# Optimization experiments

Measured on AMD Instinct MI355X. Metric: run time of the kernel, lower is better.

The kernel has to match this reference:

```python
import jax, jax.numpy as jnp
import numpy as np

HEIGHT, WIDTH = 224, 224
SIGMA = 3e-4      # soft-coverage falloff (DIB-R style delta)
EPS = 1e-10


def setup_inputs() -> dict:
    key = jax.random.key(0)
    kp, kf, kc = jax.random.split(key, 3)
    B, P, F = 2, 2048, 256
    points = 0.5 * jax.random.normal(kp, (B, P, 3), dtype=jnp.float32)
    faces = jax.random.randint(kf, (F, 3), 0, P, dtype=jnp.int32)
    colors = jax.random.uniform(kc, (B, P, 3), dtype=jnp.float32)
    rot = jnp.broadcast_to(jnp.eye(3, dtype=jnp.float32), (B, 3, 3))
    pos = jnp.tile(jnp.array([0.0, 0.0, 2.5], jnp.float32), (B, 1))
    tanfov = float(np.tan(45.0 * np.pi / 360.0))
    proj = jnp.array([[1.0 / tanfov], [1.0 / tanfov], [-1.0]], jnp.float32)
    return dict(points_bxpx3=points, faces_fx3=faces, camera_rot=rot,
                camera_pos=pos, camera_proj=proj, colors_bxpx3=colors)


def _render(points_bxpx3, camera_rot, camera_pos, camera_proj, colors_bxpx3, faces_fx3):
    H, W = HEIGHT, WIDTH
    # ---- perspective projection (kaolin DIB-R convention) ----
    pc = jnp.einsum('bpj,bij->bpi', points_bxpx3 - camera_pos[:, None, :], camera_rot)  # camera space [B,P,3]
    xyz = pc * camera_proj.reshape(1, 1, 3)
    xy = xyz[..., :2] / xyz[..., 2:3]                                   # NDC xy [B,P,2]
    i0, i1, i2 = faces_fx3[:, 0], faces_fx3[:, 1], faces_fx3[:, 2]
    p0, p1, p2 = pc[:, i0], pc[:, i1], pc[:, i2]                        # [B,F,3]
    q0, q1, q2 = xy[:, i0], xy[:, i1], xy[:, i2]                        # [B,F,2]
    normal = jnp.cross(p1 - p0, p2 - p0)                                # [B,F,3]
    normalz = normal[..., 2]
    normal1 = normal / jnp.sqrt(jnp.sum(normal * normal, -1, keepdims=True) + EPS)
    # ---- per-face vertex features: 3 verts x (rgb + mask) == color_bxfx12 ----
    ones = jnp.ones(colors_bxpx3.shape[:2] + (1,), colors_bxpx3.dtype)
    cm = jnp.concatenate([colors_bxpx3, ones], -1)                      # [B,P,4]
    feat = jnp.stack([cm[:, i0], cm[:, i1], cm[:, i2]], axis=2)         # [B,F,3,4]
    # ---- rasterize: per-pixel per-face barycentric test ----
    xs = (2.0 * jnp.arange(W, dtype=jnp.float32) + 1.0) / W - 1.0
    ys = 1.0 - (2.0 * jnp.arange(H, dtype=jnp.float32) + 1.0) / H
    PX = xs[None, None, :, None]                                        # [1,1,W,1]
    PY = ys[None, :, None, None]                                        # [1,H,1,1]
    bf = lambda a: a[:, None, None, :]                                  # [B,F] -> [B,1,1,F]
    x0, y0 = q0[..., 0], q0[..., 1]
    x1, y1 = q1[..., 0], q1[..., 1]
    x2, y2 = q2[..., 0], q2[..., 1]
    denom = (y1 - y2) * (x0 - x2) + (x2 - x1) * (y0 - y2)
    denom = jnp.where(jnp.abs(denom) < EPS, EPS, denom)
    dx2 = PX - bf(x2)
    dy2 = PY - bf(y2)
    lam0 = (bf(y1 - y2) * dx2 + bf(x2 - x1) * dy2) / bf(denom)          # [B,H,W,F]
    lam1 = (bf(y2 - y0) * dx2 + bf(x0 - x2) * dy2) / bf(denom)
    lam2 = 1.0 - lam0 - lam1
    inside = (lam0 >= 0) & (lam1 >= 0) & (lam2 >= 0)
    front = (normalz > 0)[:, None, None, :]
    valid = inside & front
    # nearest face: camera looks down -z, nearer == larger camera-space z
    zpix = lam0 * bf(p0[..., 2]) + lam1 * bf(p1[..., 2]) + lam2 * bf(p2[..., 2])
    score = jnp.where(valid, zpix, -1e10)
    idx = jnp.argmax(score, axis=-1)                                    # [B,H,W]
    valid_any = jnp.any(valid, axis=-1)
    take = lambda a: jnp.take_along_axis(a, idx[..., None], axis=-1)[..., 0]
    l0, l1, l2 = take(lam0), take(lam1), take(lam2)
    fsel = jax.vmap(lambda f, i: f[i])(feat, idx)                       # [B,H,W,3,4]
    imfeat = (l0[..., None] * fsel[..., 0, :] + l1[..., None] * fsel[..., 1, :]
              + l2[..., None] * fsel[..., 2, :]) * valid_any[..., None]
    # ---- soft coverage probability: dist to nearest edge, 0 inside ----
    def seg_d2(ax, ay, bx, by):
        ex, ey = bf(bx - ax), bf(by - ay)
        pax, pay = PX - bf(ax), PY - bf(ay)
        t = jnp.clip((pax * ex + pay * ey) / (ex * ex + ey * ey + EPS), 0.0, 1.0)
        ddx, ddy = pax - t * ex, pay - t * ey
        return ddx * ddx + ddy * ddy
    d2 = jnp.minimum(seg_d2(x0, y0, x1, y1),
                     jnp.minimum(seg_d2(x1, y1, x2, y2), seg_d2(x2, y2, x0, y0)))
    d2 = jnp.where(inside, 0.0, d2)
    prob = jnp.where(front, jnp.exp(-d2 / SIGMA) * (1.0 - 1e-7), 0.0)
    improb = (1.0 - jnp.exp(jnp.sum(jnp.log1p(-prob), axis=-1)))[..., None]  # [B,H,W,1]
    imrender = imfeat[..., :3]
    return imrender, improb, normal1


def reference(points_bxpx3, camera_rot, camera_pos, camera_proj, colors_bxpx3, faces_fx3):
    return _render(points_bxpx3, camera_rot, camera_pos, camera_proj, colors_bxpx3, faces_fx3)
```

## Files before the change

kernel.cpp:

```cpp
#include <hip/hip_runtime.h>
#include <math.h>

#define HGT 224
#define WID 224
#define NPIX (HGT * WID)
#define SIGMA 0.0003f
#define EPSV 1e-10f
#define FSTRIDE 36
#define MARGIN 0.062f


__global__ void face_pre(const float* __restrict__ points,
                         const int* __restrict__ faces,
                         const float* __restrict__ rot,
                         const float* __restrict__ pos,
                         const float* __restrict__ proj,
                         const float* __restrict__ colors,
                         float* __restrict__ fd,
                         float* __restrict__ out_normal,
                         int B, int P, int F) {
    int gid = blockIdx.x * blockDim.x + threadIdx.x;
    if (gid >= B * F) return;
    int b = gid / F;
    int f = gid - b * F;

    const float* Rb = rot + b * 9;
    float posx = pos[b * 3 + 0], posy = pos[b * 3 + 1], posz = pos[b * 3 + 2];
    float pj0 = proj[0], pj1 = proj[1], pj2 = proj[2];

    float pcx[3], pcy[3], pcz[3], qx[3], qy[3], col[9];
    for (int v = 0; v < 3; v++) {
        int i = faces[f * 3 + v];
        float dx = points[(b * P + i) * 3 + 0] - posx;
        float dy = points[(b * P + i) * 3 + 1] - posy;
        float dz = points[(b * P + i) * 3 + 2] - posz;
        pcx[v] = Rb[0] * dx + Rb[1] * dy + Rb[2] * dz;
        pcy[v] = Rb[3] * dx + Rb[4] * dy + Rb[5] * dz;
        pcz[v] = Rb[6] * dx + Rb[7] * dy + Rb[8] * dz;
        float zz = pcz[v] * pj2;
        qx[v] = (pcx[v] * pj0) / zz;
        qy[v] = (pcy[v] * pj1) / zz;
        col[v * 3 + 0] = colors[(b * P + i) * 3 + 0];
        col[v * 3 + 1] = colors[(b * P + i) * 3 + 1];
        col[v * 3 + 2] = colors[(b * P + i) * 3 + 2];
    }

    float ux = pcx[1] - pcx[0], uy = pcy[1] - pcy[0], uz = pcz[1] - pcz[0];
    float vx = pcx[2] - pcx[0], vy = pcy[2] - pcy[0], vz = pcz[2] - pcz[0];
    float nx = uy * vz - uz * vy;
    float ny = uz * vx - ux * vz;
    float nz = ux * vy - uy * vx;
    float ninv = 1.0f / sqrtf(nx * nx + ny * ny + nz * nz + EPSV);
    out_normal[gid * 3 + 0] = nx * ninv;
    out_normal[gid * 3 + 1] = ny * ninv;
    out_normal[gid * 3 + 2] = nz * ninv;

    float x0 = qx[0], y0 = qy[0], x1 = qx[1], y1 = qy[1], x2 = qx[2], y2 = qy[2];
    float denom = (y1 - y2) * (x0 - x2) + (x2 - x1) * (y0 - y2);
    if (fabsf(denom) < EPSV) denom = EPSV;
    float rd = 1.0f / denom;

    float* fp = fd + gid * FSTRIDE;
    bool front = nz > 0.0f;
    fp[0] = front ? fminf(x0, fminf(x1, x2)) :  1e30f;
    fp[1] = front ? fminf(y0, fminf(y1, y2)) :  1e30f;
    fp[2] = front ? fmaxf(x0, fmaxf(x1, x2)) : -1e30f;
    fp[3] = front ? fmaxf(y0, fmaxf(y1, y2)) : -1e30f;

    fp[4] = x0; fp[5] = y0; fp[6] = x1; fp[7] = y1; fp[8] = x2; fp[9] = y2;
    fp[10] = (y1 - y2) * rd;
    fp[11] = (x2 - x1) * rd;
    fp[12] = (y2 - y0) * rd;
    fp[13] = (x0 - x2) * rd;
    fp[14] = pcz[0]; fp[15] = pcz[1]; fp[16] = pcz[2];
    fp[17] = 0.0f;
    for (int k = 0; k < 9; k++) fp[18 + k] = col[k];

    float e01x = x1 - x0, e01y = y1 - y0;
    float e12x = x2 - x1, e12y = y2 - y1;
    float e20x = x0 - x2, e20y = y0 - y2;
    fp[27] = e01x; fp[28] = e01y; fp[29] = 1.0f / (e01x * e01x + e01y * e01y + EPSV);
    fp[30] = e12x; fp[31] = e12y; fp[32] = 1.0f / (e12x * e12x + e12y * e12y + EPSV);
    fp[33] = e20x; fp[34] = e20y; fp[35] = 1.0f / (e20x * e20x + e20y * e20y + EPSV);
}

__device__ __forceinline__ float seg_d2(float px, float py, float ax, float ay,
                                        float ex, float ey, float inv) {
    float pax = px - ax, pay = py - ay;
    float t = (pax * ex + pay * ey) * inv;
    t = fminf(fmaxf(t, 0.0f), 1.0f);
    float ddx = pax - t * ex;
    float ddy = pay - t * ey;
    return ddx * ddx + ddy * ddy;
}

__global__ __launch_bounds__(256) void rast(const float* __restrict__ fd,
                                            float* __restrict__ out,
                                            int B, int F) {
    const int tiles_x = WID / 8;
    const int tiles_per_batch = tiles_x * (HGT / 8);
    int b = blockIdx.x / tiles_per_batch;
    int tile = blockIdx.x - b * tiles_per_batch;
    int ty = tile / tiles_x;
    int tx = tile - ty * tiles_x;

    int t = threadIdx.x & 63;
    int w = threadIdx.x >> 6;
    int lx = t & 7, ly = t >> 3;
    int x = tx * 8 + lx;
    int y = ty * 8 + ly;
    float px = (2.0f * (float)x + 1.0f) / (float)WID - 1.0f;
    float py = 1.0f - (2.0f * (float)y + 1.0f) / (float)HGT;

    float txlo = (2.0f * (float)(tx * 8) + 1.0f) / (float)WID - 1.0f - MARGIN;
    float txhi = (2.0f * (float)(tx * 8 + 7) + 1.0f) / (float)WID - 1.0f + MARGIN;
    float tyhi = 1.0f - (2.0f * (float)(ty * 8) + 1.0f) / (float)HGT + MARGIN;
    float tylo = 1.0f - (2.0f * (float)(ty * 8 + 7) + 1.0f) / (float)HGT - MARGIN;

    const float* fb = fd + b * F * FSTRIDE;

    int chunk = (F + 3) >> 2;
    int fbeg = w * chunk;
    int fend = min(fbeg + chunk, F);

    float best = -1e10f;
    int bidx = -1;
    float bl0 = 0.0f, bl1 = 0.0f, bl2 = 0.0f;
    float prod = 1.0f;
    const float INSIDE_FACTOR = 1.0f - (1.0f - 1e-7f);

    for (int base = fbeg; base < fend; base += 64) {
        bool pass = false;
        int fl = base + t;
        if (fl < fend) {
            const float4 bb4 = *(const float4*)(fb + fl * FSTRIDE);
            pass = (bb4.x <= txhi) & (bb4.z >= txlo) & (bb4.y <= tyhi) & (bb4.w >= tylo);
        }
        unsigned long long mask = __ballot(pass);

        while (mask) {
            int fo = (int)__builtin_ctzll(mask);
            mask &= mask - 1;
            int fi = base + fo;
            const float* fp = fb + fi * FSTRIDE;

            float dx2 = px - fp[8], dy2 = py - fp[9];
            float lam0 = fp[10] * dx2 + fp[11] * dy2;
            float lam1 = fp[12] * dx2 + fp[13] * dy2;
            float lam2 = 1.0f - lam0 - lam1;
            bool inside = (lam0 >= 0.0f) && (lam1 >= 0.0f) && (lam2 >= 0.0f);
            unsigned long long ins = __ballot(inside);

            if (ins) {
                float zpix = lam0 * fp[14] + lam1 * fp[15] + lam2 * fp[16];
                if (inside && zpix > best) {
                    best = zpix; bidx = fi;
                    bl0 = lam0; bl1 = lam1; bl2 = lam2;
                }
            }

            if (ins == ~0ULL) {
                prod *= INSIDE_FACTOR;
            } else {
                float dA = seg_d2(px, py, fp[4], fp[5], fp[27], fp[28], fp[29]);
                float dB = seg_d2(px, py, fp[6], fp[7], fp[30], fp[31], fp[32]);
                float dC = seg_d2(px, py, fp[8], fp[9], fp[33], fp[34], fp[35]);
                float d2 = inside ? 0.0f : fminf(dA, fminf(dB, dC));
                float pr = __expf(d2 * (-1.0f / SIGMA)) * (1.0f - 1e-7f);
                prod *= (1.0f - pr);
            }
        }
    }

    __shared__ float sc[256], sl0[256], sl1[256], sl2[256], sp[256];
    __shared__ int sidx[256];
    sc[threadIdx.x] = best;
    sl0[threadIdx.x] = bl0; sl1[threadIdx.x] = bl1; sl2[threadIdx.x] = bl2;
    sp[threadIdx.x] = prod;
    sidx[threadIdx.x] = bidx;
    __syncthreads();

    if (w == 0) {
        best = -1e10f; bidx = -1;
        bl0 = 0.0f; bl1 = 0.0f; bl2 = 0.0f;
        prod = 1.0f;
        for (int k = 0; k < 4; k++) {
            int j = k * 64 + t;
            prod *= sp[j];
            float v = sc[j];
            if (v > best) {
                best = v; bidx = sidx[j];
                bl0 = sl0[j]; bl1 = sl1[j]; bl2 = sl2[j];
            }
        }

        float r = 0.0f, g = 0.0f, bb = 0.0f;
        if (bidx >= 0) {
            const float* fp = fb + bidx * FSTRIDE;
            r  = bl0 * fp[18] + bl1 * fp[21] + bl2 * fp[24];
            g  = bl0 * fp[19] + bl1 * fp[22] + bl2 * fp[25];
            bb = bl0 * fp[20] + bl1 * fp[23] + bl2 * fp[26];
        }

        int pixidx = b * NPIX + y * WID + x;
        out[pixidx * 3 + 0] = r;
        out[pixidx * 3 + 1] = g;
        out[pixidx * 3 + 2] = bb;
        out[B * NPIX * 3 + pixidx] = 1.0f - prod;
    }
}

extern "C" void kernel_launch(void* const* d_in, const int* in_sizes, int n_in,
                              void* d_out, int out_size, void* d_ws, size_t ws_size,
                              hipStream_t stream) {
    const float* points = (const float*)d_in[0];
    const int*   faces  = (const int*)d_in[1];
    const float* rot    = (const float*)d_in[2];
    const float* pos    = (const float*)d_in[3];
    const float* proj   = (const float*)d_in[4];
    const float* colors = (const float*)d_in[5];
    float* out = (float*)d_out;

    int F = in_sizes[1] / 3;
    int B = in_sizes[3] / 3;
    int P = in_sizes[0] / (3 * B);

    float* fd = (float*)d_ws;
    float* out_normal = out + B * NPIX * 3 + B * NPIX;

    int nf = B * F;
    face_pre<<<(nf + 255) / 256, 256, 0, stream>>>(points, faces, rot, pos, proj,
                                                   colors, fd, out_normal, B, P, F);

    int blocks = B * (NPIX / 64);
    rast<<<blocks, 256, 0, stream>>>(fd, out, B, F);
}
```

Baseline: 82.74 us.

## Add edge-function tile culling and split face data into filter/data buffers

Face preprocessing now writes a separate 16-float filter record holding the bounding box plus three normalized edge-line equations, and a 32-float data record in place of the 36-float one. The rasterizer culls a face for a tile when the tile center lies farther outside any edge line than the margin plus the tile half-diagonal, on top of the existing bounding-box test. This cuts the number of faces each wave processes serially in the per-face loop, for the cost of three extra float4 loads and a few FMAs per face in the filter stage. The conservative band should keep results unchanged, but it depends on the MARGIN being large enough to cover the soft-coverage falloff.

```diff
diff --git a/kernel.cpp b/kernel.cpp
--- a/kernel.cpp
+++ b/kernel.cpp
@@ -6,8 +6,11 @@
 #define NPIX (HGT * WID)
 #define SIGMA 0.0003f
 #define EPSV 1e-10f
-#define FSTRIDE 36
+#define FILT_STRIDE 16
+#define DATA_STRIDE 32
 #define MARGIN 0.062f
+#define HALFDIAG 0.04420f
+#define BAND (MARGIN + HALFDIAG)
 
 
 __global__ void face_pre(const float* __restrict__ points,
@@ -16,7 +19,8 @@
                          const float* __restrict__ pos,
                          const float* __restrict__ proj,
                          const float* __restrict__ colors,
-                         float* __restrict__ fd,
+                         float* __restrict__ filt,
+                         float* __restrict__ data,
                          float* __restrict__ out_normal,
                          int B, int P, int F) {
     int gid = blockIdx.x * blockDim.x + threadIdx.x;
@@ -60,28 +64,46 @@
     if (fabsf(denom) < EPSV) denom = EPSV;
     float rd = 1.0f / denom;
 
-    float* fp = fd + gid * FSTRIDE;
+    float a00 = (y1 - y2) * rd;
+    float a01 = (x2 - x1) * rd;
+    float a10 = (y2 - y0) * rd;
+    float a11 = (x0 - x2) * rd;
+
+    float* fq = filt + gid * FILT_STRIDE;
     bool front = nz > 0.0f;
-    fp[0] = front ? fminf(x0, fminf(x1, x2)) :  1e30f;
-    fp[1] = front ? fminf(y0, fminf(y1, y2)) :  1e30f;
-    fp[2] = front ? fmaxf(x0, fmaxf(x1, x2)) : -1e30f;
-    fp[3] = front ? fmaxf(y0, fmaxf(y1, y2)) : -1e30f;
-
-    fp[4] = x0; fp[5] = y0; fp[6] = x1; fp[7] = y1; fp[8] = x2; fp[9] = y2;
-    fp[10] = (y1 - y2) * rd;
-    fp[11] = (x2 - x1) * rd;
-    fp[12] = (y2 - y0) * rd;
-    fp[13] = (x0 - x2) * rd;
-    fp[14] = pcz[0]; fp[15] = pcz[1]; fp[16] = pcz[2];
-    fp[17] = 0.0f;
-    for (int k = 0; k < 9; k++) fp[18 + k] = col[k];
+    fq[0] = front ? fminf(x0, fminf(x1, x2)) :  1e30f;
+    fq[1] = front ? fminf(y0, fminf(y1, y2)) :  1e30f;
+    fq[2] = front ? fmaxf(x0, fmaxf(x1, x2)) : -1e30f;
+    fq[3] = front ? fmaxf(y0, fmaxf(y1, y2)) : -1e30f;
+
+    float n0 = 1.0f / sqrtf(a00 * a00 + a01 * a01 + EPSV);
+    float n1 = 1.0f / sqrtf(a10 * a10 + a11 * a11 + EPSV);
+    float g2x = -(a00 + a10), g2y = -(a01 + a11);
+    float n2 = 1.0f / sqrtf(g2x * g2x + g2y * g2y + EPSV);
+    fq[4] = a00 * n0;
+    fq[5] = a01 * n0;
+    fq[6] = -(a00 * x2 + a01 * y2) * n0;
+    fq[7] = a10 * n1;
+    fq[8] = a11 * n1;
+    fq[9] = -(a10 * x2 + a11 * y2) * n1;
+    fq[10] = g2x * n2;
+    fq[11] = g2y * n2;
+    fq[12] = (1.0f - g2x * x2 - g2y * y2) * n2;
+    fq[13] = 0.0f; fq[14] = 0.0f; fq[15] = 0.0f;
+
+    float* fp = data + gid * DATA_STRIDE;
+    fp[0] = x0; fp[1] = y0; fp[2] = x1; fp[3] = y1; fp[4] = x2; fp[5] = y2;
+    fp[6] = a00; fp[7] = a01; fp[8] = a10; fp[9] = a11;
+    fp[10] = pcz[0]; fp[11] = pcz[1]; fp[12] = pcz[2];
+    fp[13] = 0.0f;
+    for (int k = 0; k < 9; k++) fp[14 + k] = col[k];
 
     float e01x = x1 - x0, e01y = y1 - y0;
     float e12x = x2 - x1, e12y = y2 - y1;
     float e20x = x0 - x2, e20y = y0 - y2;
-    fp[27] = e01x; fp[28] = e01y; fp[29] = 1.0f / (e01x * e01x + e01y * e01y + EPSV);
-    fp[30] = e12x; fp[31] = e12y; fp[32] = 1.0f / (e12x * e12x + e12y * e12y + EPSV);
-    fp[33] = e20x; fp[34] = e20y; fp[35] = 1.0f / (e20x * e20x + e20y * e20y + EPSV);
+    fp[23] = e01x; fp[24] = e01y; fp[25] = 1.0f / (e01x * e01x + e01y * e01y + EPSV);
+    fp[26] = e12x; fp[27] = e12y; fp[28] = 1.0f / (e12x * e12x + e12y * e12y + EPSV);
+    fp[29] = e20x; fp[30] = e20y; fp[31] = 1.0f / (e20x * e20x + e20y * e20y + EPSV);
 }
 
 __device__ __forceinline__ float seg_d2(float px, float py, float ax, float ay,
@@ -94,7 +116,8 @@
     return ddx * ddx + ddy * ddy;
 }
 
-__global__ __launch_bounds__(256) void rast(const float* __restrict__ fd,
+__global__ __launch_bounds__(256) void rast(const float* __restrict__ filt,
+                                            const float* __restrict__ data,
                                             float* __restrict__ out,
                                             int B, int F) {
     const int tiles_x = WID / 8;
@@ -116,8 +139,11 @@
     float txhi = (2.0f * (float)(tx * 8 + 7) + 1.0f) / (float)WID - 1.0f + MARGIN;
     float tyhi = 1.0f - (2.0f * (float)(ty * 8) + 1.0f) / (float)HGT + MARGIN;
     float tylo = 1.0f - (2.0f * (float)(ty * 8 + 7) + 1.0f) / (float)HGT - MARGIN;
-
-    const float* fb = fd + b * F * FSTRIDE;
+    float cx = (16.0f * (float)tx + 8.0f) / (float)WID - 1.0f;
+    float cy = 1.0f - (16.0f * (float)ty + 8.0f) / (float)HGT;
+
+    const float* fltb = filt + (size_t)b * F * FILT_STRIDE;
+    const float* datb = data + (size_t)b * F * DATA_STRIDE;
 
     int chunk = (F + 3) >> 2;
     int fbeg = w * chunk;
@@ -133,8 +159,16 @@
         bool pass = false;
         int fl = base + t;
         if (fl < fend) {
-            const float4 bb4 = *(const float4*)(fb + fl * FSTRIDE);
-            pass = (bb4.x <= txhi) & (bb4.z >= txlo) & (bb4.y <= tyhi) & (bb4.w >= tylo);
+            const float* fq = fltb + fl * FILT_STRIDE;
+            float4 bb = *(const float4*)fq;
+            float4 e0 = *(const float4*)(fq + 4);
+            float4 e1 = *(const float4*)(fq + 8);
+            float  dc2 = fq[12];
+            bool bpass = (bb.x <= txhi) & (bb.z >= txlo) & (bb.y <= tyhi) & (bb.w >= tylo);
+            float d0 = e0.x * cx + e0.y * cy + e0.z;
+            float d1 = e0.w * cx + e1.x * cy + e1.y;
+            float d2 = e1.z * cx + e1.w * cy + dc2;
+            pass = bpass & (fminf(d0, fminf(d1, d2)) >= -BAND);
         }
         unsigned long long mask = __ballot(pass);
 
@@ -142,17 +176,17 @@
             int fo = (int)__builtin_ctzll(mask);
             mask &= mask - 1;
             int fi = base + fo;
-            const float* fp = fb + fi * FSTRIDE;
-
-            float dx2 = px - fp[8], dy2 = py - fp[9];
-            float lam0 = fp[10] * dx2 + fp[11] * dy2;
-            float lam1 = fp[12] * dx2 + fp[13] * dy2;
+            const float* fp = datb + fi * DATA_STRIDE;
+
+            float dx2 = px - fp[4], dy2 = py - fp[5];
+            float lam0 = fp[6] * dx2 + fp[7] * dy2;
+            float lam1 = fp[8] * dx2 + fp[9] * dy2;
             float lam2 = 1.0f - lam0 - lam1;
             bool inside = (lam0 >= 0.0f) && (lam1 >= 0.0f) && (lam2 >= 0.0f);
             unsigned long long ins = __ballot(inside);
 
             if (ins) {
-                float zpix = lam0 * fp[14] + lam1 * fp[15] + lam2 * fp[16];
+                float zpix = lam0 * fp[10] + lam1 * fp[11] + lam2 * fp[12];
                 if (inside && zpix > best) {
                     best = zpix; bidx = fi;
                     bl0 = lam0; bl1 = lam1; bl2 = lam2;
@@ -162,9 +196,9 @@
             if (ins == ~0ULL) {
                 prod *= INSIDE_FACTOR;
             } else {
-                float dA = seg_d2(px, py, fp[4], fp[5], fp[27], fp[28], fp[29]);
-                float dB = seg_d2(px, py, fp[6], fp[7], fp[30], fp[31], fp[32]);
-                float dC = seg_d2(px, py, fp[8], fp[9], fp[33], fp[34], fp[35]);
+                float dA = seg_d2(px, py, fp[0], fp[1], fp[23], fp[24], fp[25]);
+                float dB = seg_d2(px, py, fp[2], fp[3], fp[26], fp[27], fp[28]);
+                float dC = seg_d2(px, py, fp[4], fp[5], fp[29], fp[30], fp[31]);
                 float d2 = inside ? 0.0f : fminf(dA, fminf(dB, dC));
                 float pr = __expf(d2 * (-1.0f / SIGMA)) * (1.0f - 1e-7f);
                 prod *= (1.0f - pr);
@@ -196,10 +230,10 @@
 
         float r = 0.0f, g = 0.0f, bb = 0.0f;
         if (bidx >= 0) {
-            const float* fp = fb + bidx * FSTRIDE;
-            r  = bl0 * fp[18] + bl1 * fp[21] + bl2 * fp[24];
-            g  = bl0 * fp[19] + bl1 * fp[22] + bl2 * fp[25];
-            bb = bl0 * fp[20] + bl1 * fp[23] + bl2 * fp[26];
+            const float* fp = datb + bidx * DATA_STRIDE;
+            r  = bl0 * fp[14] + bl1 * fp[17] + bl2 * fp[20];
+            g  = bl0 * fp[15] + bl1 * fp[18] + bl2 * fp[21];
+            bb = bl0 * fp[16] + bl1 * fp[19] + bl2 * fp[22];
         }
 
         int pixidx = b * NPIX + y * WID + x;
@@ -225,13 +259,15 @@
     int B = in_sizes[3] / 3;
     int P = in_sizes[0] / (3 * B);
 
-    float* fd = (float*)d_ws;
+    float* filt = (float*)d_ws;
+    float* data = filt + (size_t)B * F * FILT_STRIDE;
     float* out_normal = out + B * NPIX * 3 + B * NPIX;
 
     int nf = B * F;
     face_pre<<<(nf + 255) / 256, 256, 0, stream>>>(points, faces, rot, pos, proj,
-                                                   colors, fd, out_normal, B, P, F);
+                                                   colors, filt, data, out_normal,
+                                                   B, P, F);
 
     int blocks = B * (NPIX / 64);
-    rast<<<blocks, 256, 0, stream>>>(fd, out, B, F);
-}
+    rast<<<blocks, 256, 0, stream>>>(filt, data, out, B, F);
+}
```

Measured after the change: 80.98 us. 1.02x faster.
